# Kernel optimization log

Measured on AMD Instinct MI355X. Metric: run time of the kernel, lower is better.

## Reference

```python
import jax, jax.numpy as jnp
import numpy as np

K = 16
CIN = 128
COUT = 128
EPS = 1e-5
SLOPE = 0.01  # default negative_slope of nn.LeakyReLU


def _bn(w, gamma, beta):
    # BatchNorm1d in training mode over channel axis (last): stats over (N, k)
    mean = jnp.mean(w, axis=(0, 1))
    var = jnp.var(w, axis=(0, 1))  # biased variance, as torch uses for normalization
    return (w - mean) * jax.lax.rsqrt(var + EPS) * gamma + beta


def _leaky(x):
    return jnp.where(x >= 0, x, SLOPE * x)


def setup_inputs() -> dict:
    key = jax.random.key(0)
    ks = jax.random.split(key, 10)
    N = 8192
    s = 0.05
    return {
        "fea_i": jax.random.normal(ks[0], (N, CIN), jnp.float32),
        "fea_last": jax.random.normal(ks[1], (N, CIN), jnp.float32),
        "xyz_i": jax.random.uniform(ks[2], (N, 3), jnp.float32),
        "xyz_last": jax.random.uniform(ks[3], (N, 3), jnp.float32),
        "batch": jnp.zeros((N,), jnp.int32),
        "Wq": jax.random.normal(ks[4], (COUT, CIN), jnp.float32) * s,
        "bq": jnp.zeros((COUT,), jnp.float32),
        "Wk": jax.random.normal(ks[5], (COUT, CIN), jnp.float32) * s,
        "bk": jnp.zeros((COUT,), jnp.float32),
        "Wv": jax.random.normal(ks[6], (COUT, CIN), jnp.float32) * s,
        "bv": jnp.zeros((COUT,), jnp.float32),
        "bn1_gamma": jnp.ones((COUT,), jnp.float32),
        "bn1_beta": jnp.zeros((COUT,), jnp.float32),
        "Wl": jax.random.normal(ks[7], (COUT, COUT), jnp.float32) * s,
        "bl": jnp.zeros((COUT,), jnp.float32),
        "bn2_gamma": jnp.ones((COUT,), jnp.float32),
        "bn2_beta": jnp.zeros((COUT,), jnp.float32),
    }


def reference(fea_i, fea_last, xyz_i, xyz_last, batch, Wq, bq, Wk, bk, Wv, bv,
              bn1_gamma, bn1_beta, Wl, bl, bn2_gamma, bn2_beta):
    # knn: for each point in xyz_last, K nearest neighbors in xyz_i (single batch)
    d2 = jnp.sum((xyz_last[:, None, :] - xyz_i[None, :, :]) ** 2, axis=-1)  # (N, N)
    _, idx = jax.lax.top_k(-d2, K)  # (N, K) indices into xyz_i / fea_i

    fk = fea_i[idx]                                   # (N, K, CIN) gathered neighbor feats
    q = fea_last @ Wq.T + bq                          # (N, COUT); fea_last[idx_last] == row-repeat
    kk = jnp.einsum('nkc,oc->nko', fk, Wk) + bk       # (N, K, COUT)
    w = q[:, None, :] - kk                            # (N, K, COUT)

    # lin_w: BN -> LeakyReLU -> Linear -> BN -> LeakyReLU
    w = _leaky(_bn(w, bn1_gamma, bn1_beta))
    w = jnp.einsum('nko,po->nkp', w, Wl) + bl
    w = _leaky(_bn(w, bn2_gamma, bn2_beta))

    w = jax.nn.softmax(w, axis=1)                     # softmax over K neighbors
    v = jnp.einsum('nkc,oc->nko', fk, Wv) + bv        # (N, K, COUT)
    return jnp.sum(w * v, axis=1)                     # (N, COUT)
```

## Files before the change

### kernel.cpp

```cpp
#include <hip/hip_runtime.h>
#include <stdint.h>

#define NPTS   8192
#define NROWS  (NPTS * 16)
#define SLOPE  0.01f
#define BN_EPS 1e-5f

#define TP     0.13f
#define TP2    (TP * TP)
#define LDEP   6
#define LSTR   7
#define TF     0.2f
#define TF2    0.04f
#define CAPF   408
#define EPSB   1e-5f

#define OFF_Q      0u
#define OFF_KP     4194304u
#define OFF_VP     8388608u
#define OFF_STATS  12582912u
#define OFF_TAB    12845056u
#define OFF_IDX    13041664u
#define OFF_BIG    13585408u
#define WS_NEED    47139840u

#define T_PCNT 0
#define T_POFF 512
#define T_PCUR 1025

typedef __bf16 bf16x8 __attribute__((ext_vector_type(8)));
typedef float  f32x4  __attribute__((ext_vector_type(4)));

__device__ __forceinline__ unsigned int pack_bf2(float lo, float hi) {
  unsigned int a = __float_as_uint(lo);
  unsigned int b = __float_as_uint(hi);
  unsigned int ra = (a + 0x7fffu + ((a >> 16) & 1u)) >> 16;
  unsigned int rb = (b + 0x7fffu + ((b >> 16) & 1u)) & 0xffff0000u;
  return ra | rb;
}
__device__ __forceinline__ unsigned short bf1(float v) {
  unsigned int a = __float_as_uint(v);
  return (unsigned short)((a + 0x7fffu + ((a >> 16) & 1u)) >> 16);
}
__device__ __forceinline__ float bf2f(unsigned short u) {
  return __uint_as_float(((unsigned int)u) << 16);
}

__device__ __forceinline__ int cell_of(float x, float y, float z) {
  int cx = min(7, max(0, (int)(x * 8.f)));
  int cy = min(7, max(0, (int)(y * 8.f)));
  int cz = min(7, max(0, (int)(z * 8.f)));
  return (cz * 8 + cy) * 8 + cx;
}

__device__ __forceinline__ void insert16(unsigned long long* key, unsigned long long kk) {
  if (kk < key[15]) {
    #pragma unroll
    for (int u = 15; u >= 1; --u) {
      bool cm1 = kk < key[u - 1];
      bool cs  = kk < key[u];
      key[u] = cm1 ? key[u - 1] : (cs ? kk : key[u]);
    }
    key[0] = (kk < key[0]) ? kk : key[0];
  }
}

template<int D>
__device__ __forceinline__ void tournament16(unsigned long long (&lst)[D], int lane,
                                             int* __restrict__ sidxq, int* __restrict__ idxoq) {
  int myidx = 0;
  #pragma unroll 1
  for (int r = 0; r < 16; ++r) {
    const float hd = __uint_as_float((unsigned int)(lst[0] >> 32));
    float wm = hd;
    #pragma unroll
    for (int o = 32; o; o >>= 1) wm = fminf(wm, __shfl_xor(wm, o));
    bool iswin = (hd == wm);
    const unsigned long long wmask = __ballot(iswin);
    unsigned int widx;
    if (__popcll(wmask) > 1) {
      unsigned int mi = iswin ? (unsigned int)lst[0] : 0xffffffffu;
      #pragma unroll
      for (int o = 32; o; o >>= 1) {
        unsigned int u = (unsigned int)__shfl_xor((int)mi, o);
        mi = (u < mi) ? u : mi;
      }
      widx = mi;
      iswin = iswin && ((unsigned int)lst[0] == mi);
    } else {
      const int wl = (int)__builtin_ctzll(wmask);
      widx = (unsigned int)__builtin_amdgcn_readlane((int)(unsigned int)lst[0], wl);
    }
    #pragma unroll
    for (int u = 0; u < D - 1; ++u) lst[u] = iswin ? lst[u + 1] : lst[u];
    lst[D - 1] = iswin ? ~0ull : lst[D - 1];
    if (lane == r) myidx = (int)widx;
  }
  if (lane < 16) { idxoq[lane] = myidx; sidxq[lane] = myidx; }
}

template<int D>
__device__ __forceinline__ void extract_topk(const unsigned long long* __restrict__ poolq, int n, int lane,
                                             int* __restrict__ sidxq, int* __restrict__ idxoq) {
  unsigned long long lst[D];
  #pragma unroll
  for (int j = 0; j < D; ++j) lst[j] = ~0ull;
  for (int j = lane; j < n; j += 64) {
    unsigned long long kk = poolq[j];
    #pragma unroll
    for (int u = D - 1; u >= 1; --u) {
      bool cm1 = kk < lst[u - 1];
      bool cs  = kk < lst[u];
      lst[u] = cm1 ? lst[u - 1] : (cs ? kk : lst[u]);
    }
    lst[0] = (kk < lst[0]) ? kk : lst[0];
  }
  tournament16<D>(lst, lane, sidxq, idxoq);
}

__device__ __forceinline__ int scan_ball(const int* __restrict__ poff, const float4* __restrict__ bp,
                                         float qx, float qy, float qz, float rad, float r2, int cap,
                                         unsigned long long* __restrict__ poolw,
                                         int lane, unsigned long long below) {
  const int lx = max(0, (int)floorf((qx - rad - EPSB) * 8.f));
  const int hx = min(7, (int)floorf((qx + rad + EPSB) * 8.f));
  const int ly = max(0, (int)floorf((qy - rad - EPSB) * 8.f));
  const int hy = min(7, (int)floorf((qy + rad + EPSB) * 8.f));
  const int lz = max(0, (int)floorf((qz - rad - EPSB) * 8.f));
  const int hz = min(7, (int)floorf((qz + rad + EPSB) * 8.f));
  const int nrY = hy - ly + 1, nrows = nrY * (hz - lz + 1);
  int zi = 0;
  #pragma unroll
  for (int z2 = 1; z2 < 5; ++z2) zi += (lane >= z2 * nrY) ? 1 : 0;
  const int yi = lane - zi * nrY;
  int rs = 0, re = 0;
  if (lane < nrows) {
    const int crow = ((lz + zi) * 8 + (ly + yi)) * 8;
    rs = poff[crow + lx]; re = poff[crow + hx + 1];
  }
  int cnt = 0;
  for (int r = 0; r < nrows; ++r) {
    const int rsr = __builtin_amdgcn_readlane(rs, r);
    const int rer = __builtin_amdgcn_readlane(re, r);
    for (int base = rsr; base < rer; base += 64) {
      const int pos = base + lane;
      const float4 pp = bp[pos];
      float dx = qx - pp.x, dy = qy - pp.y, dz = qz - pp.z;
      float dd = fmaf(dx, dx, fmaf(dy, dy, dz * dz));
      bool g = (pos < rer) && (dd < r2);
      unsigned long long mask = __ballot(g);
      int p2 = cnt + (int)__popcll(mask & below);
      if (g && p2 < cap)
        poolw[p2] = ((unsigned long long)__float_as_uint(dd) << 32) | (unsigned int)__float_as_int(pp.w);
      cnt += (int)__popcll(mask);
    }
  }
  return cnt;
}

__global__ __launch_bounds__(256) void k_zero(int* __restrict__ tab,
                                              float* __restrict__ stats,
                                              float4* __restrict__ bp) {
  const int T = blockIdx.x * 256 + threadIdx.x;
  if (T < 8192) stats[T] = 0.f;
  if (T < 512)  tab[T_PCNT + T] = 0;
  if (T < 64)   bp[NPTS + T] = make_float4(1e9f, 1e9f, 1e9f, __int_as_float(0));
}

__global__ __launch_bounds__(256) void k_count(const float* __restrict__ xyz_i,
                                               int* __restrict__ tab) {
  const int t = blockIdx.x * 256 + threadIdx.x;
  atomicAdd(&tab[T_PCNT + cell_of(xyz_i[t * 3], xyz_i[t * 3 + 1], xyz_i[t * 3 + 2])], 1);
}

__global__ __launch_bounds__(512) void k_offsets(int* __restrict__ tab) {
  __shared__ int ls[512];
  const int t = threadIdx.x;
  const int v = tab[T_PCNT + t];
  ls[t] = v;
  __syncthreads();
  for (int ofs = 1; ofs < 512; ofs <<= 1) {
    int add = (t >= ofs) ? ls[t - ofs] : 0;
    __syncthreads();
    ls[t] += add;
    __syncthreads();
  }
  tab[T_POFF + t] = ls[t] - v;
  tab[T_PCUR + t] = ls[t] - v;
  if (t == 511) tab[T_POFF + 512] = ls[511];
}

__global__ __launch_bounds__(256) void k_scatter(const float* __restrict__ xyz_i,
                                                 int* __restrict__ tab,
                                                 float4* __restrict__ bp) {
  const int t = blockIdx.x * 256 + threadIdx.x;
  float x = xyz_i[t * 3], y = xyz_i[t * 3 + 1], z = xyz_i[t * 3 + 2];
  int pos = atomicAdd(&tab[T_PCUR + cell_of(x, y, z)], 1);
  bp[pos] = make_float4(x, y, z, __int_as_float(t));
}

__global__ __launch_bounds__(256) void k_proj(const float* __restrict__ fea_i,
                                              const float* __restrict__ fea_last,
                                              const float* __restrict__ Wq,
                                              const float* __restrict__ Wk,
                                              const float* __restrict__ Wv,
                                              const float* __restrict__ bq,
                                              const float* __restrict__ bk,
                                              const float* __restrict__ bv,
                                              float* __restrict__ Qo,
                                              float* __restrict__ Kpo,
                                              float* __restrict__ Vpo) {
  const int z = blockIdx.y;
  const float* A    = (z == 0) ? fea_last : fea_i;
  const float* W    = (z == 0) ? Wq : ((z == 1) ? Wk : Wv);
  const float* bias = (z == 0) ? bq : ((z == 1) ? bk : bv);
  float* Out        = (z == 0) ? Qo : ((z == 1) ? Kpo : Vpo);

  __shared__ unsigned short wl[128 * 128];
  const int t = threadIdx.x;
  const int lane = t & 63, w = t >> 6;

  #pragma unroll
  for (int i = 0; i < 8; ++i) {
    const int chunk = i * 256 + t;
    const int p = chunk >> 4, cseg = chunk & 15;
    const float4 wa = *(const float4*)(W + (size_t)p * 128 + cseg * 8);
    const float4 wb = *(const float4*)(W + (size_t)p * 128 + cseg * 8 + 4);
    uint4 pk;
    pk.x = pack_bf2(wa.x, wa.y); pk.y = pack_bf2(wa.z, wa.w);
    pk.z = pack_bf2(wb.x, wb.y); pk.w = pack_bf2(wb.z, wb.w);
    *(uint4*)((char*)wl + p * 256 + ((cseg * 16) ^ ((p & 7) << 4))) = pk;
  }
  __syncthreads();

  const int rowtile = blockIdx.x * 64 + w * 16;
  const int kslot = lane & 15, kgrp = lane >> 4;
  const float* Arow = A + (size_t)(rowtile + kslot) * 128;

  f32x4 acc[8];
  #pragma unroll
  for (int tt = 0; tt < 8; ++tt) acc[tt] = (f32x4){0.f, 0.f, 0.f, 0.f};

  #pragma unroll
  for (int s = 0; s < 4; ++s) {
    const int c0 = s * 32 + kgrp * 8;
    const float4 qa = *(const float4*)(Arow + c0);
    const float4 qb = *(const float4*)(Arow + c0 + 4);
    uint4 af;
    af.x = pack_bf2(qa.x, qa.y); af.y = pack_bf2(qa.z, qa.w);
    af.z = pack_bf2(qb.x, qb.y); af.w = pack_bf2(qb.z, qb.w);
    const bf16x8 Af = __builtin_bit_cast(bf16x8, af);
    const int cbyte = s * 64 + kgrp * 16;
    #pragma unroll
    for (int tt = 0; tt < 8; ++tt) {
      const int prow = tt * 16 + kslot;
      const uint4 bw = *(const uint4*)((const char*)wl + prow * 256 + (cbyte ^ ((prow & 7) << 4)));
      acc[tt] = __builtin_amdgcn_mfma_f32_16x16x32_bf16(Af, __builtin_bit_cast(bf16x8, bw), acc[tt], 0, 0, 0);
    }
  }

  #pragma unroll
  for (int tt = 0; tt < 8; ++tt) {
    const int col = tt * 16 + kslot;
    const float bb = bias[col];
    #pragma unroll
    for (int r = 0; r < 4; ++r) {
      const int row = rowtile + kgrp * 4 + r;
      Out[(size_t)row * 128 + col] = acc[tt][r] + bb;
    }
  }
}

__global__ __launch_bounds__(256) void k_knn(const int* __restrict__ tab,
                                             const float4* __restrict__ bp,
                                             const float* __restrict__ xyz_last,
                                             const float* __restrict__ Q,
                                             const float* __restrict__ Kp,
                                             int* __restrict__ idxo,
                                             float* __restrict__ st1) {
  __shared__ unsigned long long pool[4][64 * LSTR];
  __shared__ int sidx[4][16];
  __shared__ float red[4][256];
  const int t = threadIdx.x, lane = t & 63, wave = t >> 6;
  const int q = blockIdx.x * 4 + wave;
  const float qx = xyz_last[q * 3];
  const float qy = xyz_last[q * 3 + 1];
  const float qz = xyz_last[q * 3 + 2];
  const int* poff = &tab[T_POFF];
  const unsigned long long below = (1ull << lane) - 1ull;

  unsigned long long* myslots = &pool[wave][lane * LSTR];
  int cnt = 0;
  {
    const int lx = max(0, (int)floorf((qx - TP - EPSB) * 8.f));
    const int hx = min(7, (int)floorf((qx + TP + EPSB) * 8.f));
    const int ly = max(0, (int)floorf((qy - TP - EPSB) * 8.f));
    const int hy = min(7, (int)floorf((qy + TP + EPSB) * 8.f));
    const int lz = max(0, (int)floorf((qz - TP - EPSB) * 8.f));
    const int hz = min(7, (int)floorf((qz + TP + EPSB) * 8.f));
    const int nrY = hy - ly + 1, nrows = nrY * (hz - lz + 1);
    int zi = 0;
    #pragma unroll
    for (int z2 = 1; z2 < 5; ++z2) zi += (lane >= z2 * nrY) ? 1 : 0;
    const int yi = lane - zi * nrY;
    int rs = 0, re = 0;
    if (lane < nrows) {
      const int crow = ((lz + zi) * 8 + (ly + yi)) * 8;
      rs = poff[crow + lx]; re = poff[crow + hx + 1];
    }
    for (int r = 0; r < nrows; ++r) {
      const int rsr = __builtin_amdgcn_readlane(rs, r);
      const int rer = __builtin_amdgcn_readlane(re, r);
      #pragma unroll 2
      for (int base = rsr; base < rer; base += 64) {
        const int pos = base + lane;
        const float4 pp = bp[pos];
        float dx = qx - pp.x, dy = qy - pp.y, dz = qz - pp.z;
        float dd = fmaf(dx, dx, fmaf(dy, dy, dz * dz));
        if ((pos < rer) && (dd < TP2)) {
          if (cnt < LDEP)
            myslots[cnt] = ((unsigned long long)__float_as_uint(dd) << 32) | (unsigned int)__float_as_int(pp.w);
          ++cnt;
        }
      }
    }
  }
  const bool anyover = __ballot(cnt > LDEP) != 0ull;
  int tot = cnt;
  #pragma unroll
  for (int o = 32; o; o >>= 1) tot += __shfl_xor(tot, o);

  if (!anyover && tot >= 16) {
    unsigned long long lst[LDEP];
    #pragma unroll
    for (int j = 0; j < LDEP; ++j) lst[j] = ~0ull;
    for (int j = 0; j < cnt; ++j) {
      unsigned long long kk = myslots[j];
      #pragma unroll
      for (int u = LDEP - 1; u >= 1; --u) {
        bool cm1 = kk < lst[u - 1];
        bool cs  = kk < lst[u];
        lst[u] = cm1 ? lst[u - 1] : (cs ? kk : lst[u]);
      }
      lst[0] = (kk < lst[0]) ? kk : lst[0];
    }
    tournament16<LDEP>(lst, lane, &sidx[wave][0], &idxo[q * 16]);
  } else {
    unsigned long long* flat = &pool[wave][0];
    int c1 = scan_ball(poff, bp, qx, qy, qz, TF, TF2, CAPF, flat, lane, below);
    if (c1 >= 16 && c1 <= CAPF) {
      extract_topk<7>(flat, c1, lane, &sidx[wave][0], &idxo[q * 16]);
    } else {
      unsigned long long key[16];
      #pragma unroll
      for (int u = 0; u < 16; ++u) key[u] = ~0ull;
      for (int it = 0; it < NPTS / 64; ++it) {
        const float4 pp = bp[it * 64 + lane];
        float dx = qx - pp.x, dy = qy - pp.y, dz = qz - pp.z;
        float dd = fmaf(dx, dx, fmaf(dy, dy, dz * dz));
        insert16(key, ((unsigned long long)__float_as_uint(dd) << 32) | (unsigned int)__float_as_int(pp.w));
      }
      unsigned long long myout = ~0ull;
      #pragma unroll 1
      for (int r = 0; r < 16; ++r) {
        unsigned long long w = key[0];
        #pragma unroll
        for (int o = 32; o; o >>= 1) {
          unsigned long long u = __shfl_xor(w, o);
          w = (u < w) ? u : w;
        }
        if (key[0] == w) {
          #pragma unroll
          for (int u = 0; u < 15; ++u) key[u] = key[u + 1];
          key[15] = ~0ull;
        }
        if (lane == r) myout = w;
      }
      if (lane < 16) {
        idxo[q * 16 + lane] = (int)(myout & 0xffffffffull);
        sidx[wave][lane] = (int)(myout & 0xffffffffull);
      }
    }
  }

  const int c0 = lane * 2;
  const float2 qv = *(const float2*)(Q + (size_t)q * 128 + c0);
  float s0 = 0.f, s1 = 0.f, v0 = 0.f, v1 = 0.f;
  #pragma unroll 4
  for (int k = 0; k < 16; ++k) {
    const int pid = sidx[wave][k];
    const float2 kv = *(const float2*)(Kp + (size_t)pid * 128 + c0);
    const float w0 = qv.x - kv.x, w1 = qv.y - kv.y;
    s0 += w0; v0 += w0 * w0;
    s1 += w1; v1 += w1 * w1;
  }
  red[wave][c0]       = s0;  red[wave][c0 + 1]   = s1;
  red[wave][128 + c0] = v0;  red[wave][129 + c0] = v1;
  __syncthreads();
  {
    const float totv = red[0][t & 255] + red[1][t & 255] + red[2][t & 255] + red[3][t & 255];
    atomicAdd(&st1[(blockIdx.x & 15) * 256 + (t & 255)], totv);
  }
}

__global__ void k_bnfin(const float* __restrict__ stats, int nrep, float invM,
                        const float* __restrict__ gamma, const float* __restrict__ beta,
                        float* __restrict__ bn) {
  const int o = threadIdx.x;
  float s = 0.f, q = 0.f;
  for (int r = 0; r < nrep; ++r) { s += stats[r * 256 + o]; q += stats[r * 256 + 128 + o]; }
  float mean = s * invM;
  float var  = fmaf(-mean, mean, q * invM);
  float sc = gamma[o] * rsqrtf(var + BN_EPS);
  bn[o]       = sc;
  bn[128 + o] = fmaf(-mean, sc, beta[o]);
}

__global__ __launch_bounds__(256) void k_mid(const float* __restrict__ Q,
                                             const float* __restrict__ Kp,
                                             const int* __restrict__ idx,
                                             const float* __restrict__ Wl,
                                             const float* __restrict__ bl,
                                             const float* __restrict__ bn1,
                                             float* __restrict__ stats2,
                                             unsigned short* __restrict__ Y) {
  __shared__ union {
    unsigned short wl[128 * 128];
    struct {
      unsigned short stage[64][136];
      float red[4 * 256];
    } ep;
  } sm;

  const int t = threadIdx.x;
  const int lane = t & 63, w = t >> 6;
  const int rowbase = blockIdx.x * 64;

  #pragma unroll
  for (int i = 0; i < 8; ++i) {
    const int chunk = i * 256 + t;
    const int p = chunk >> 4, cseg = chunk & 15;
    const float4 wa = *(const float4*)(Wl + (size_t)p * 128 + cseg * 8);
    const float4 wb = *(const float4*)(Wl + (size_t)p * 128 + cseg * 8 + 4);
    uint4 pk;
    pk.x = pack_bf2(wa.x, wa.y); pk.y = pack_bf2(wa.z, wa.w);
    pk.z = pack_bf2(wb.x, wb.y); pk.w = pack_bf2(wb.z, wb.w);
    *(uint4*)((char*)sm.wl + p * 256 + ((cseg * 16) ^ ((p & 7) << 4))) = pk;
  }
  __syncthreads();

  const int n = blockIdx.x * 4 + w;
  const int kslot = lane & 15;
  const int kgrp  = lane >> 4;
  const int pid = idx[n * 16 + kslot];
  const float* Qrow = Q + (size_t)n * 128;
  const float* Krow = Kp + (size_t)pid * 128;

  f32x4 acc[8];
  #pragma unroll
  for (int tt = 0; tt < 8; ++tt) acc[tt] = (f32x4){0.f, 0.f, 0.f, 0.f};

  #pragma unroll
  for (int s = 0; s < 4; ++s) {
    const int c0 = s * 32 + kgrp * 8;
    const float4 qa = *(const float4*)(Qrow + c0);
    const float4 qb = *(const float4*)(Qrow + c0 + 4);
    const float4 ka = *(const float4*)(Krow + c0);
    const float4 kb = *(const float4*)(Krow + c0 + 4);
    const float4 sa = *(const float4*)(bn1 + c0);
    const float4 sb = *(const float4*)(bn1 + c0 + 4);
    const float4 ha = *(const float4*)(bn1 + 128 + c0);
    const float4 hb = *(const float4*)(bn1 + 128 + c0 + 4);
    float x[8];
    x[0] = fmaf(qa.x - ka.x, sa.x, ha.x);
    x[1] = fmaf(qa.y - ka.y, sa.y, ha.y);
    x[2] = fmaf(qa.z - ka.z, sa.z, ha.z);
    x[3] = fmaf(qa.w - ka.w, sa.w, ha.w);
    x[4] = fmaf(qb.x - kb.x, sb.x, hb.x);
    x[5] = fmaf(qb.y - kb.y, sb.y, hb.y);
    x[6] = fmaf(qb.z - kb.z, sb.z, hb.z);
    x[7] = fmaf(qb.w - kb.w, sb.w, hb.w);
    uint4 af;
    af.x = pack_bf2(fmaxf(x[0], SLOPE * x[0]), fmaxf(x[1], SLOPE * x[1]));
    af.y = pack_bf2(fmaxf(x[2], SLOPE * x[2]), fmaxf(x[3], SLOPE * x[3]));
    af.z = pack_bf2(fmaxf(x[4], SLOPE * x[4]), fmaxf(x[5], SLOPE * x[5]));
    af.w = pack_bf2(fmaxf(x[6], SLOPE * x[6]), fmaxf(x[7], SLOPE * x[7]));
    const bf16x8 A = __builtin_bit_cast(bf16x8, af);
    const int cbyte = s * 64 + kgrp * 16;
    #pragma unroll
    for (int tt = 0; tt < 8; ++tt) {
      const int prow = tt * 16 + kslot;
      const uint4 bw = *(const uint4*)((const char*)sm.wl + prow * 256 + (cbyte ^ ((prow & 7) << 4)));
      acc[tt] = __builtin_amdgcn_mfma_f32_16x16x32_bf16(A, __builtin_bit_cast(bf16x8, bw), acc[tt], 0, 0, 0);
    }
  }
  __syncthreads();

  #pragma unroll
  for (int tt = 0; tt < 8; ++tt) {
    const int col = tt * 16 + kslot;
    const float bb = bl[col];
    float s = 0.f, q2 = 0.f;
    #pragma unroll
    for (int r = 0; r < 4; ++r) {
      const float v = acc[tt][r] + bb;
      s += v; q2 += v * v;
      sm.ep.stage[w * 16 + kgrp * 4 + r][col] = bf1(v);
    }
    s  += __shfl_xor(s, 16);  s  += __shfl_xor(s, 32);
    q2 += __shfl_xor(q2, 16); q2 += __shfl_xor(q2, 32);
    if (kgrp == 0) {
      sm.ep.red[w * 256 + col]       = s;
      sm.ep.red[w * 256 + 128 + col] = q2;
    }
  }
  __syncthreads();

  #pragma unroll
  for (int i = 0; i < 4; ++i) {
    const int chunk = i * 256 + t;
    const int row = chunk >> 4, cc = chunk & 15;
    const uint4 v = *(const uint4*)&sm.ep.stage[row][cc * 8];
    *(uint4*)&Y[(size_t)(rowbase + row) * 128 + cc * 8] = v;
  }
  {
    const float tot = sm.ep.red[t] + sm.ep.red[256 + t] + sm.ep.red[512 + t] + sm.ep.red[768 + t];
    atomicAdd(&stats2[(blockIdx.x & 15) * 256 + t], tot);
  }
}

__global__ __launch_bounds__(128) void k_epi(const unsigned short* __restrict__ Y,
                                             const float* __restrict__ Vp,
                                             const int* __restrict__ idx,
                                             const float* __restrict__ bn2,
                                             float* __restrict__ out) {
  const int n = blockIdx.x;
  const int p = threadIdx.x;
  const float s2 = bn2[p], sh2 = bn2[128 + p];
  float z[16];
  #pragma unroll
  for (int k = 0; k < 16; ++k) {
    float yv = bf2f(Y[(size_t)(n * 16 + k) * 128 + p]);
    float v = fmaf(yv, s2, sh2);
    z[k] = (v >= 0.f) ? v : SLOPE * v;
  }
  float m = z[0];
  #pragma unroll
  for (int k = 1; k < 16; ++k) m = fmaxf(m, z[k]);
  float acc = 0.f, denom = 0.f;
  #pragma unroll
  for (int k = 0; k < 16; ++k) {
    float e = __expf(z[k] - m);
    denom += e;
    const int pid = idx[n * 16 + k];
    acc = fmaf(e, Vp[(size_t)pid * 128 + p], acc);
  }
  out[(size_t)n * 128 + p] = acc / denom;
}

extern "C" void kernel_launch(void* const* d_in, const int* in_sizes, int n_in,
                              void* d_out, int out_size, void* d_ws, size_t ws_size,
                              hipStream_t stream) {
  const float* fea_i    = (const float*)d_in[0];
  const float* fea_last = (const float*)d_in[1];
  const float* xyz_i    = (const float*)d_in[2];
  const float* xyz_last = (const float*)d_in[3];
  const float* Wq = (const float*)d_in[5];
  const float* bq = (const float*)d_in[6];
  const float* Wk = (const float*)d_in[7];
  const float* bk = (const float*)d_in[8];
  const float* Wv = (const float*)d_in[9];
  const float* bv = (const float*)d_in[10];
  const float* g1 = (const float*)d_in[11];
  const float* b1 = (const float*)d_in[12];
  const float* Wl = (const float*)d_in[13];
  const float* bl = (const float*)d_in[14];
  const float* g2 = (const float*)d_in[15];
  const float* b2 = (const float*)d_in[16];

  if (ws_size < (size_t)WS_NEED) return;

  char* ws = (char*)d_ws;
  float*  Q      = (float*)(ws + OFF_Q);
  float*  Kp     = (float*)(ws + OFF_KP);
  float*  Vp     = (float*)(ws + OFF_VP);
  int*    tab    = (int*)  (ws + OFF_TAB);
  int*    idxb   = (int*)  (ws + OFF_IDX);
  float*  st1    = (float*)(ws + OFF_STATS);
  float*  st2    = st1 + 4096;
  float*  bn1    = st1 + 8192;
  float*  bn2    = st1 + 8448;
  float4* bp     = (float4*)(ws + OFF_BIG);
  unsigned short* Y = (unsigned short*)(ws + OFF_BIG);

  k_zero<<<33, 256, 0, stream>>>(tab, st1, bp);
  k_proj<<<dim3(128, 3), 256, 0, stream>>>(fea_i, fea_last, Wq, Wk, Wv, bq, bk, bv, Q, Kp, Vp);
  k_count<<<32, 256, 0, stream>>>(xyz_i, tab);
  k_offsets<<<1, 512, 0, stream>>>(tab);
  k_scatter<<<32, 256, 0, stream>>>(xyz_i, tab, bp);
  k_knn<<<2048, 256, 0, stream>>>(tab, bp, xyz_last, Q, Kp, idxb, st1);
  k_bnfin<<<1, 128, 0, stream>>>(st1, 16, 1.f / (float)NROWS, g1, b1, bn1);
  k_mid<<<2048, 256, 0, stream>>>(Q, Kp, idxb, Wl, bl, bn1, st2, Y);
  k_bnfin<<<1, 128, 0, stream>>>(st2, 16, 1.f / (float)NROWS, g2, b2, bn2);
  k_epi<<<8192, 128, 0, stream>>>(Y, Vp, idxb, bn2, (float*)d_out);
}
```

Before: 116.9 us.

## Fuse grid binning into one block and fold BN finalize into consumers

Merges zeroing, cell counting, prefix scan and scatter into a single 1024-thread block that uses shared-memory atomics. The separate BN finalize kernels are removed, and each k_mid/k_epi block now recomputes the BN scale and shift from the partial stats. This cuts the launch count from ten to five to reduce launch overhead and inter-kernel gaps. The cost is some redundant stat reduction per block (16 loads per channel per block) and a serial single-block binning stage.

```diff
diff --git a/kernel.cpp b/kernel.cpp
--- a/kernel.cpp
+++ b/kernel.cpp
@@ -5,6 +5,7 @@
 #define NROWS  (NPTS * 16)
 #define SLOPE  0.01f
 #define BN_EPS 1e-5f
+#define INVM   (1.f / (float)NROWS)
 
 #define TP     0.13f
 #define TP2    (TP * TP)
@@ -24,9 +25,7 @@
 #define OFF_BIG    13585408u
 #define WS_NEED    47139840u
 
-#define T_PCNT 0
-#define T_POFF 512
-#define T_PCUR 1025
+#define T_POFF 0
 
 typedef __bf16 bf16x8 __attribute__((ext_vector_type(8)));
 typedef float  f32x4  __attribute__((ext_vector_type(4)));
@@ -158,45 +157,48 @@
   return cnt;
 }
 
-__global__ __launch_bounds__(256) void k_zero(int* __restrict__ tab,
+__global__ __launch_bounds__(1024) void k_bin(const float* __restrict__ xyz_i,
+                                              int* __restrict__ tab,
                                               float* __restrict__ stats,
                                               float4* __restrict__ bp) {
-  const int T = blockIdx.x * 256 + threadIdx.x;
-  if (T < 8192) stats[T] = 0.f;
-  if (T < 512)  tab[T_PCNT + T] = 0;
-  if (T < 64)   bp[NPTS + T] = make_float4(1e9f, 1e9f, 1e9f, __int_as_float(0));
-}
-
-__global__ __launch_bounds__(256) void k_count(const float* __restrict__ xyz_i,
-                                               int* __restrict__ tab) {
-  const int t = blockIdx.x * 256 + threadIdx.x;
-  atomicAdd(&tab[T_PCNT + cell_of(xyz_i[t * 3], xyz_i[t * 3 + 1], xyz_i[t * 3 + 2])], 1);
-}
-
-__global__ __launch_bounds__(512) void k_offsets(int* __restrict__ tab) {
-  __shared__ int ls[512];
+  __shared__ int cnt[512];
+  __shared__ int scn[512];
   const int t = threadIdx.x;
-  const int v = tab[T_PCNT + t];
-  ls[t] = v;
+  #pragma unroll
+  for (int i = 0; i < 8; ++i) stats[i * 1024 + t] = 0.f;
+  if (t < 512) cnt[t] = 0;
+  if (t < 64)  bp[NPTS + t] = make_float4(1e9f, 1e9f, 1e9f, __int_as_float(0));
+  __syncthreads();
+
+  float xs[8], ys[8], zs[8]; int cl[8];
+  #pragma unroll
+  for (int i = 0; i < 8; ++i) {
+    const int p = i * 1024 + t;
+    xs[i] = xyz_i[p * 3]; ys[i] = xyz_i[p * 3 + 1]; zs[i] = xyz_i[p * 3 + 2];
+    cl[i] = cell_of(xs[i], ys[i], zs[i]);
+    atomicAdd(&cnt[cl[i]], 1);
+  }
+  __syncthreads();
+
+  if (t < 512) scn[t] = cnt[t];
   __syncthreads();
   for (int ofs = 1; ofs < 512; ofs <<= 1) {
-    int add = (t >= ofs) ? ls[t - ofs] : 0;
+    int add = (t < 512 && t >= ofs) ? scn[t - ofs] : 0;
     __syncthreads();
-    ls[t] += add;
+    if (t < 512) scn[t] += add;
     __syncthreads();
   }
-  tab[T_POFF + t] = ls[t] - v;
-  tab[T_PCUR + t] = ls[t] - v;
-  if (t == 511) tab[T_POFF + 512] = ls[511];
-}
-
-__global__ __launch_bounds__(256) void k_scatter(const float* __restrict__ xyz_i,
-                                                 int* __restrict__ tab,
-                                                 float4* __restrict__ bp) {
-  const int t = blockIdx.x * 256 + threadIdx.x;
-  float x = xyz_i[t * 3], y = xyz_i[t * 3 + 1], z = xyz_i[t * 3 + 2];
-  int pos = atomicAdd(&tab[T_PCUR + cell_of(x, y, z)], 1);
-  bp[pos] = make_float4(x, y, z, __int_as_float(t));
+  if (t < 512) tab[T_POFF + t] = scn[t] - cnt[t];
+  if (t == 511) tab[T_POFF + 512] = scn[511];
+  __syncthreads();
+  if (t < 512) scn[t] -= cnt[t];
+  __syncthreads();
+
+  #pragma unroll
+  for (int i = 0; i < 8; ++i) {
+    const int pos = atomicAdd(&scn[cl[i]], 1);
+    bp[pos] = make_float4(xs[i], ys[i], zs[i], __int_as_float(i * 1024 + t));
+  }
 }
 
 __global__ __launch_bounds__(256) void k_proj(const float* __restrict__ fea_i,
@@ -403,25 +405,14 @@
   }
 }
 
-__global__ void k_bnfin(const float* __restrict__ stats, int nrep, float invM,
-                        const float* __restrict__ gamma, const float* __restrict__ beta,
-                        float* __restrict__ bn) {
-  const int o = threadIdx.x;
-  float s = 0.f, q = 0.f;
-  for (int r = 0; r < nrep; ++r) { s += stats[r * 256 + o]; q += stats[r * 256 + 128 + o]; }
-  float mean = s * invM;
-  float var  = fmaf(-mean, mean, q * invM);
-  float sc = gamma[o] * rsqrtf(var + BN_EPS);
-  bn[o]       = sc;
-  bn[128 + o] = fmaf(-mean, sc, beta[o]);
-}
-
 __global__ __launch_bounds__(256) void k_mid(const float* __restrict__ Q,
                                              const float* __restrict__ Kp,
                                              const int* __restrict__ idx,
                                              const float* __restrict__ Wl,
                                              const float* __restrict__ bl,
-                                             const float* __restrict__ bn1,
+                                             const float* __restrict__ st1,
+                                             const float* __restrict__ g1,
+                                             const float* __restrict__ b1,
                                              float* __restrict__ stats2,
                                              unsigned short* __restrict__ Y) {
   __shared__ union {
@@ -431,6 +422,7 @@
       float red[4 * 256];
     } ep;
   } sm;
+  __shared__ float bn1s[256];
 
   const int t = threadIdx.x;
   const int lane = t & 63, w = t >> 6;
@@ -447,6 +439,16 @@
     pk.z = pack_bf2(wb.x, wb.y); pk.w = pack_bf2(wb.z, wb.w);
     *(uint4*)((char*)sm.wl + p * 256 + ((cseg * 16) ^ ((p & 7) << 4))) = pk;
   }
+  if (t < 128) {
+    float s = 0.f, q2 = 0.f;
+    #pragma unroll
+    for (int r = 0; r < 16; ++r) { s += st1[r * 256 + t]; q2 += st1[r * 256 + 128 + t]; }
+    const float mean = s * INVM;
+    const float var  = fmaf(-mean, mean, q2 * INVM);
+    const float sc = g1[t] * rsqrtf(var + BN_EPS);
+    bn1s[t]       = sc;
+    bn1s[128 + t] = fmaf(-mean, sc, b1[t]);
+  }
   __syncthreads();
 
   const int n = blockIdx.x * 4 + w;
@@ -467,10 +469,10 @@
     const float4 qb = *(const float4*)(Qrow + c0 + 4);
     const float4 ka = *(const float4*)(Krow + c0);
     const float4 kb = *(const float4*)(Krow + c0 + 4);
-    const float4 sa = *(const float4*)(bn1 + c0);
-    const float4 sb = *(const float4*)(bn1 + c0 + 4);
-    const float4 ha = *(const float4*)(bn1 + 128 + c0);
-    const float4 hb = *(const float4*)(bn1 + 128 + c0 + 4);
+    const float4 sa = *(const float4*)(bn1s + c0);
+    const float4 sb = *(const float4*)(bn1s + c0 + 4);
+    const float4 ha = *(const float4*)(bn1s + 128 + c0);
+    const float4 hb = *(const float4*)(bn1s + 128 + c0 + 4);
     float x[8];
     x[0] = fmaf(qa.x - ka.x, sa.x, ha.x);
     x[1] = fmaf(qa.y - ka.y, sa.y, ha.y);
@@ -532,11 +534,20 @@
 __global__ __launch_bounds__(128) void k_epi(const unsigned short* __restrict__ Y,
                                              const float* __restrict__ Vp,
                                              const int* __restrict__ idx,
-                                             const float* __restrict__ bn2,
+                                             const float* __restrict__ st2,
+                                             const float* __restrict__ g2,
+                                             const float* __restrict__ b2,
                                              float* __restrict__ out) {
   const int n = blockIdx.x;
   const int p = threadIdx.x;
-  const float s2 = bn2[p], sh2 = bn2[128 + p];
+  float s = 0.f, q2 = 0.f;
+  #pragma unroll
+  for (int r = 0; r < 16; ++r) { s += st2[r * 256 + p]; q2 += st2[r * 256 + 128 + p]; }
+  const float mean = s * INVM;
+  const float var  = fmaf(-mean, mean, q2 * INVM);
+  const float s2 = g2[p] * rsqrtf(var + BN_EPS);
+  const float sh2 = fmaf(-mean, s2, b2[p]);
+
   float z[16];
   #pragma unroll
   for (int k = 0; k < 16; ++k) {
@@ -588,19 +599,12 @@
   int*    idxb   = (int*)  (ws + OFF_IDX);
   float*  st1    = (float*)(ws + OFF_STATS);
   float*  st2    = st1 + 4096;
-  float*  bn1    = st1 + 8192;
-  float*  bn2    = st1 + 8448;
   float4* bp     = (float4*)(ws + OFF_BIG);
   unsigned short* Y = (unsigned short*)(ws + OFF_BIG);
 
-  k_zero<<<33, 256, 0, stream>>>(tab, st1, bp);
+  k_bin<<<1, 1024, 0, stream>>>(xyz_i, tab, st1, bp);
   k_proj<<<dim3(128, 3), 256, 0, stream>>>(fea_i, fea_last, Wq, Wk, Wv, bq, bk, bv, Q, Kp, Vp);
-  k_count<<<32, 256, 0, stream>>>(xyz_i, tab);
-  k_offsets<<<1, 512, 0, stream>>>(tab);
-  k_scatter<<<32, 256, 0, stream>>>(xyz_i, tab, bp);
   k_knn<<<2048, 256, 0, stream>>>(tab, bp, xyz_last, Q, Kp, idxb, st1);
-  k_bnfin<<<1, 128, 0, stream>>>(st1, 16, 1.f / (float)NROWS, g1, b1, bn1);
-  k_mid<<<2048, 256, 0, stream>>>(Q, Kp, idxb, Wl, bl, bn1, st2, Y);
-  k_bnfin<<<1, 128, 0, stream>>>(st2, 16, 1.f / (float)NROWS, g2, b2, bn2);
-  k_epi<<<8192, 128, 0, stream>>>(Y, Vp, idxb, bn2, (float*)d_out);
-}
+  k_mid<<<2048, 256, 0, stream>>>(Q, Kp, idxb, Wl, bl, st1, g1, b1, st2, Y);
+  k_epi<<<8192, 128, 0, stream>>>(Y, Vp, idxb, st2, g2, b2, (float*)d_out);
+}
```

Measured after the change: 104.3 us. -10.8%, faster.
